# Performance work log

Hardware: AMD Instinct MI355X
Metric: run time of the kernel (lower is better)

The kernel has to match this reference:

```python
import jax, jax.numpy as jnp
import numpy as np

N_EMBD = 768

def setup_inputs() -> dict:
    key = jax.random.key(0)
    k1, k2, k3, k4 = jax.random.split(key, 4)
    B, T, head_size = 16, 1024, 128
    x = jax.random.normal(k1, (B, T, N_EMBD), dtype=jnp.float32)
    # nn.Linear(in, out, bias=False): weight stored as (out, in); we store transposed (in, out)
    s = 1.0 / np.sqrt(N_EMBD)
    Wk = jax.random.uniform(k2, (N_EMBD, head_size), jnp.float32, -s, s)
    Wq = jax.random.uniform(k3, (N_EMBD, head_size), jnp.float32, -s, s)
    Wv = jax.random.uniform(k4, (N_EMBD, head_size), jnp.float32, -s, s)
    return {"x": x, "Wk": Wk, "Wq": Wq, "Wv": Wv}

def reference(x, Wk, Wq, Wv):
    B, T, C = x.shape  # C == n_embd == 768
    k = jnp.einsum('btc,ch->bth', x, Wk)
    q = jnp.einsum('btc,ch->bth', x, Wq)
    v = jnp.einsum('btc,ch->bth', x, Wv)
    # NOTE: original scales by C**-0.5 with C = n_embd (768), not head_size.
    wei = jnp.einsum('bth,bsh->bts', q, k) * (C ** -0.5)  # (B, T, T)
    causal = jnp.tril(jnp.ones((T, T), dtype=bool))
    wei = jnp.where(causal, wei, -jnp.inf)
    wei = jax.nn.softmax(wei, axis=-1)
    # dropout p=0.0 -> identity
    return jnp.einsum('bts,bsh->bth', wei, v)
```

## Files before the change

kernel.cpp:

```cpp
#include <hip/hip_runtime.h>
#include <math.h>

#define NTOK   16384
#define NEMBD  768
#define HDIM   128

typedef __attribute__((ext_vector_type(8)))  short short8;
typedef __attribute__((ext_vector_type(16))) float floatx16;

#define MFMA32(a,b,c) __builtin_amdgcn_mfma_f32_32x32x16_bf16(a,b,c,0,0,0)

__device__ __forceinline__ unsigned short f2bf(float f) {
    unsigned u = __float_as_uint(f);
    u += 0x7fff + ((u >> 16) & 1);
    return (unsigned short)(u >> 16);
}
__device__ __forceinline__ unsigned pack2(float a, float b) {
    return (unsigned)f2bf(a) | ((unsigned)f2bf(b) << 16);
}
__device__ __forceinline__ unsigned pack2_trunc(float a, float b) {
    return __builtin_amdgcn_perm(__float_as_uint(b), __float_as_uint(a),
                                 0x07060302u);
}
__device__ __forceinline__ void gl_lds16(const void* gptr, void* lptr) {
    __builtin_amdgcn_global_load_lds(
        (const __attribute__((address_space(1))) unsigned int*)gptr,
        (__attribute__((address_space(3))) unsigned int*)lptr, 16, 0, 0);
}

__global__ __launch_bounds__(256) void prep_w(
    const float* __restrict__ Wk, const float* __restrict__ Wq,
    const float* __restrict__ Wv, unsigned short* __restrict__ wt)
{
    __shared__ float T[64 * 65];

    const int tid = threadIdx.x;
    const int bw  = blockIdx.x / 24;
    const int rem = blockIdx.x % 24;
    const int ct  = rem >> 1, dh = rem & 1;
    const int c0  = ct * 64, d0 = dh * 64;
    const float* W = (bw == 0) ? Wk : ((bw == 1) ? Wq : Wv);
    const float scale = (bw == 1)
        ? (0.03608439182435161f * 1.4426950408889634f) : 1.0f;

    #pragma unroll
    for (int pass = 0; pass < 4; ++pass) {
        int idx = pass * 256 + tid;
        int c  = idx >> 4;
        int d4 = idx & 15;
        float4 v = ((const float4*)W)[(size_t)(c0 + c) * 32 + dh * 16 + d4];
        v.x *= scale; v.y *= scale; v.z *= scale; v.w *= scale;
        T[(d4 * 4 + 0) * 65 + c] = v.x;
        T[(d4 * 4 + 1) * 65 + c] = v.y;
        T[(d4 * 4 + 2) * 65 + c] = v.z;
        T[(d4 * 4 + 3) * 65 + c] = v.w;
    }
    __syncthreads();

    #pragma unroll
    for (int pass = 0; pass < 2; ++pass) {
        int idx = pass * 256 + tid;
        int d  = idx >> 3;
        int c8 = idx & 7;
        const float* row = &T[d * 65 + c8 * 8];
        uint4 u = make_uint4(pack2(row[0], row[1]), pack2(row[2], row[3]),
                             pack2(row[4], row[5]), pack2(row[6], row[7]));
        *(uint4*)&wt[(size_t)bw * (HDIM * NEMBD) + (size_t)(d0 + d) * NEMBD
                     + c0 + c8 * 8] = u;
    }
}

__global__ __launch_bounds__(256) void qkv_fused(
    const float* __restrict__ x, const unsigned short* __restrict__ wt,
    unsigned short* __restrict__ kb, unsigned short* __restrict__ qb,
    unsigned short* __restrict__ vT)
{
    __shared__ __align__(16) char As[2][8192];
    __shared__ __align__(16) char Bs[2][24576];

    const int tid = threadIdx.x, w = tid >> 6, lane = tid & 63;
    const int l31 = lane & 31, h = lane >> 5;
    const int r8 = lane >> 3, c8 = lane & 7;
    const int wm = w >> 1, wn = w & 1;
    const int mtile = blockIdx.x >> 1, nh = blockIdx.x & 1;
    const int m0 = mtile * 64;
    const int nbase = nh * 192;
    const int arow = tid >> 2, ac = tid & 3;

    floatx16 acc[3];
    #pragma unroll
    for (int j = 0; j < 3; ++j)
        #pragma unroll
        for (int i = 0; i < 16; ++i) acc[j][i] = 0.f;

    const float* asrc = x + (size_t)(m0 + arow) * NEMBD + ac * 16;

    #pragma unroll
    for (int j = 0; j < 6; ++j) {
        int rowb = w * 48 + j * 8;
        int row  = rowb + r8;
        gl_lds16((const char*)wt + ((size_t)(nbase + row) * NEMBD) * 2
                     + ((c8 ^ (row & 7)) * 16),
                 Bs[0] + rowb * 128);
    }
    float4 a0 = ((const float4*)asrc)[0];
    float4 a1 = ((const float4*)asrc)[1];
    float4 a2 = ((const float4*)asrc)[2];
    float4 a3 = ((const float4*)asrc)[3];
    {
        uint4 u0 = make_uint4(pack2(a0.x, a0.y), pack2(a0.z, a0.w),
                              pack2(a1.x, a1.y), pack2(a1.z, a1.w));
        uint4 u1 = make_uint4(pack2(a2.x, a2.y), pack2(a2.z, a2.w),
                              pack2(a3.x, a3.y), pack2(a3.z, a3.w));
        int cA = 2 * ac, cB = 2 * ac + 1;
        *(uint4*)(As[0] + arow * 128 + ((cA ^ (arow & 7)) * 16)) = u0;
        *(uint4*)(As[0] + arow * 128 + ((cB ^ (arow & 7)) * 16)) = u1;
    }
    {
        const float4* src = (const float4*)(asrc + 64);
        a0 = src[0]; a1 = src[1]; a2 = src[2]; a3 = src[3];
    }
    __syncthreads();

    #pragma unroll
    for (int it = 0; it < 12; ++it) {
        char* Acur = As[it & 1];
        char* Bcur = Bs[it & 1];
        char* Anxt = As[(it & 1) ^ 1];
        char* Bnxt = Bs[(it & 1) ^ 1];

        if (it < 11) {
            const int k0n = (it + 1) * 64;
            #pragma unroll
            for (int j = 0; j < 6; ++j) {
                int rowb = w * 48 + j * 8;
                int row  = rowb + r8;
                gl_lds16((const char*)wt
                             + ((size_t)(nbase + row) * NEMBD + k0n) * 2
                             + ((c8 ^ (row & 7)) * 16),
                         Bnxt + rowb * 128);
            }
        }

        #pragma unroll
        for (int ks = 0; ks < 4; ++ks) {
            int ar = wm * 32 + l31;
            short8 af = *(const short8*)(Acur + ar * 128
                                         + (((2*ks + h) ^ (ar & 7)) * 16));
            #pragma unroll
            for (int j = 0; j < 3; ++j) {
                int br = wn * 96 + j * 32 + l31;
                short8 bf = *(const short8*)(Bcur + br * 128
                                             + (((2*ks + h) ^ (br & 7)) * 16));
                acc[j] = MFMA32(af, bf, acc[j]);
            }
        }

        if (it < 11) {
            uint4 u0 = make_uint4(pack2(a0.x, a0.y), pack2(a0.z, a0.w),
                                  pack2(a1.x, a1.y), pack2(a1.z, a1.w));
            uint4 u1 = make_uint4(pack2(a2.x, a2.y), pack2(a2.z, a2.w),
                                  pack2(a3.x, a3.y), pack2(a3.z, a3.w));
            int cA = 2 * ac, cB = 2 * ac + 1;
            *(uint4*)(Anxt + arow * 128 + ((cA ^ (arow & 7)) * 16)) = u0;
            *(uint4*)(Anxt + arow * 128 + ((cB ^ (arow & 7)) * 16)) = u1;
            if (it < 10) {
                const float4* src = (const float4*)(asrc + (it + 2) * 64);
                a0 = src[0]; a1 = src[1]; a2 = src[2]; a3 = src[3];
            }
        }
        __syncthreads();
    }

    const int tbase = m0 + wm * 32;
    #pragma unroll
    for (int j = 0; j < 3; ++j) {
        int n0 = nbase + wn * 96 + j * 32;
        if (n0 < 256) {
            unsigned short* outp = (n0 < 128) ? kb : qb;
            int d = (n0 & 127) + l31;
            #pragma unroll
            for (int r = 0; r < 16; ++r) {
                int t = tbase + (r & 3) + 8 * (r >> 2) + 4 * h;
                outp[(size_t)t * HDIM + d] = f2bf(acc[j][r]);
            }
        } else {
            int d = (n0 - 256) + l31, b = m0 >> 10, tloc = (m0 & 1023) + wm * 32;
            #pragma unroll
            for (int g = 0; g < 4; ++g) {
                int t = tloc + 8 * g + 4 * h;
                uint2 u = make_uint2(pack2(acc[j][4*g+0], acc[j][4*g+1]),
                                     pack2(acc[j][4*g+2], acc[j][4*g+3]));
                *(uint2*)((char*)vT + (((size_t)(b * HDIM + d)) * 1024 + t) * 2) = u;
            }
        }
    }
}

__global__ __launch_bounds__(256) void attn_mfma(
    const unsigned short* __restrict__ qb, const unsigned short* __restrict__ kb,
    const unsigned short* __restrict__ vT, float* __restrict__ out)
{
    __shared__ __align__(16) float Obuf[4 * 32 * 128];
    __shared__ float lred[128];

    const int tid = threadIdx.x, w = tid >> 6, lane = tid & 63;
    const int l31 = lane & 31, h = lane >> 5;
    const int u  = blockIdx.x & 255;
    const int b  = u & 15, p = u >> 4;
    const int qt = (blockIdx.x >> 8) ? (31 - p) : p;

    const char* kb_b = (const char*)kb + (size_t)b * (1024 * 256);
    const char* qb_b = (const char*)qb + (size_t)b * (1024 * 256);
    const char* vT_b = (const char*)vT + (size_t)b * (HDIM * 2048);

    short8 qf[8];
    {
        const char* qrow = qb_b + (size_t)(qt * 32 + l31) * 256 + h * 16;
        #pragma unroll
        for (int ks = 0; ks < 8; ++ks)
            qf[ks] = *(const short8*)(qrow + ks * 32);
    }

    floatx16 o[4];
    #pragma unroll
    for (int nt = 0; nt < 4; ++nt)
        #pragma unroll
        for (int i = 0; i < 16; ++i) o[nt][i] = 0.f;
    float l_r = 0.f;

    short8 kf[8];
    if (w <= qt) {
        const char* krow = kb_b + (size_t)(w * 32 + l31) * 256 + h * 16;
        #pragma unroll
        for (int ks = 0; ks < 8; ++ks)
            kf[ks] = *(const short8*)(krow + ks * 32);
    }

    for (int st = w; st <= qt; st += 4) {
        short8 vf[8];
        {
            const char* vrow0 = vT_b + (size_t)l31 * 2048 + (size_t)st * 64 + h * 16;
            #pragma unroll
            for (int nt = 0; nt < 4; ++nt) {
                const char* vr = vrow0 + (size_t)nt * (32 * 2048);
                vf[nt * 2 + 0] = *(const short8*)(vr + 0);
                vf[nt * 2 + 1] = *(const short8*)(vr + 32);
            }
        }
        floatx16 s;
        #pragma unroll
        for (int i = 0; i < 16; ++i) s[i] = 0.f;
        __builtin_amdgcn_s_setprio(1);
        #pragma unroll
        for (int ks = 0; ks < 8; ++ks) s = MFMA32(kf[ks], qf[ks], s);
        __builtin_amdgcn_s_setprio(0);

        if (st + 4 <= qt) {
            const char* krow = kb_b + (size_t)((st + 4) * 32 + l31) * 256 + h * 16;
            #pragma unroll
            for (int ks = 0; ks < 8; ++ks)
                kf[ks] = *(const short8*)(krow + ks * 32);
        }

        if (st == qt) {
            #pragma unroll
            for (int r = 0; r < 16; ++r) {
                int key = (r & 3) + 8 * (r >> 2) + 4 * h;
                if (key > l31) s[r] = -1e30f;
            }
        }
        float p16[16];
        float ps0 = 0.f, ps1 = 0.f, ps2 = 0.f, ps3 = 0.f;
        #pragma unroll
        for (int r = 0; r < 4; ++r) {
            p16[4*r+0] = __builtin_amdgcn_exp2f(s[4*r+0]);
            p16[4*r+1] = __builtin_amdgcn_exp2f(s[4*r+1]);
            p16[4*r+2] = __builtin_amdgcn_exp2f(s[4*r+2]);
            p16[4*r+3] = __builtin_amdgcn_exp2f(s[4*r+3]);
            ps0 += p16[4*r+0]; ps1 += p16[4*r+1];
            ps2 += p16[4*r+2]; ps3 += p16[4*r+3];
        }
        l_r += (ps0 + ps1) + (ps2 + ps3);

        unsigned own[8];
        #pragma unroll
        for (int i = 0; i < 8; ++i) own[i] = pack2_trunc(p16[2*i], p16[2*i+1]);
        asm("v_permlane32_swap_b32 %0, %1" : "+v"(own[0]), "+v"(own[2]));
        asm("v_permlane32_swap_b32 %0, %1" : "+v"(own[1]), "+v"(own[3]));
        asm("v_permlane32_swap_b32 %0, %1" : "+v"(own[4]), "+v"(own[6]));
        asm("v_permlane32_swap_b32 %0, %1" : "+v"(own[5]), "+v"(own[7]));
        short8 pf[2];
        {
            union { short8 v; unsigned uu[4]; } f0, f1;
            f0.uu[0]=own[0]; f0.uu[1]=own[1]; f0.uu[2]=own[2]; f0.uu[3]=own[3];
            f1.uu[0]=own[4]; f1.uu[1]=own[5]; f1.uu[2]=own[6]; f1.uu[3]=own[7];
            pf[0] = f0.v; pf[1] = f1.v;
        }
        __builtin_amdgcn_s_setprio(1);
        #pragma unroll
        for (int nt = 0; nt < 4; ++nt) {
            o[nt] = MFMA32(vf[nt * 2 + 0], pf[0], o[nt]);
            o[nt] = MFMA32(vf[nt * 2 + 1], pf[1], o[nt]);
        }
        __builtin_amdgcn_s_setprio(0);
    }

    l_r += __shfl_xor(l_r, 32, 64);
    if (lane < 32) lred[w * 32 + l31] = l_r;
    {
        float* mybuf = &Obuf[w * 4096];
        #pragma unroll
        for (int nt = 0; nt < 4; ++nt) {
            #pragma unroll
            for (int g = 0; g < 4; ++g) {
                int chunk = nt * 8 + 2 * g + h;
                int slot  = (chunk & 24) | ((chunk & 7) ^ (l31 & 7));
                *((float4*)&mybuf[l31 * 128] + slot) =
                    make_float4(o[nt][4*g+0], o[nt][4*g+1],
                                o[nt][4*g+2], o[nt][4*g+3]);
            }
        }
    }
    __syncthreads();
    {
        int q  = tid >> 3;
        int cb = (tid & 7) * 4;
        float inv = 1.f / (lred[q] + lred[32 + q] + lred[64 + q] + lred[96 + q]);
        #pragma unroll
        for (int cc = 0; cc < 4; ++cc) {
            int chunk = cb + cc;
            int slot  = (chunk & 24) | ((chunk & 7) ^ (q & 7));
            float4 v0 = *((float4*)&Obuf[0 * 4096 + q * 128] + slot);
            float4 v1 = *((float4*)&Obuf[1 * 4096 + q * 128] + slot);
            float4 v2 = *((float4*)&Obuf[2 * 4096 + q * 128] + slot);
            float4 v3 = *((float4*)&Obuf[3 * 4096 + q * 128] + slot);
            float4 v = make_float4((v0.x + v1.x + v2.x + v3.x) * inv,
                                   (v0.y + v1.y + v2.y + v3.y) * inv,
                                   (v0.z + v1.z + v2.z + v3.z) * inv,
                                   (v0.w + v1.w + v2.w + v3.w) * inv);
            *(float4*)&out[((size_t)(b * 1024 + qt * 32 + q)) * HDIM + chunk * 4] = v;
        }
    }
}

extern "C" void kernel_launch(void* const* d_in, const int* in_sizes, int n_in,
                              void* d_out, int out_size, void* d_ws, size_t ws_size,
                              hipStream_t stream)
{
    const float* x  = (const float*)d_in[0];
    const float* Wk = (const float*)d_in[1];
    const float* Wq = (const float*)d_in[2];
    const float* Wv = (const float*)d_in[3];
    float* outp = (float*)d_out;

    char* ws = (char*)d_ws;
    unsigned short* wt = (unsigned short*)(ws);
    unsigned short* kb = (unsigned short*)(ws + 589824);
    unsigned short* qb = (unsigned short*)(ws + 4784128);
    unsigned short* vT = (unsigned short*)(ws + 8978432);

    prep_w<<<72, 256, 0, stream>>>(Wk, Wq, Wv, wt);
    qkv_fused<<<512, 256, 0, stream>>>(x, wt, kb, qb, vT);
    attn_mfma<<<512, 256, 0, stream>>>(qb, kb, vT, outp);
}
```

Baseline: 125.3 us.

## Load x fragments directly into registers, bypassing LDS staging in QKV GEMM

The QKV projection kernel no longer stages the fp32 x tile through shared memory. Each lane now loads its own MFMA A-fragment straight from global memory into registers, one k-step ahead, and converts it to bf16 in place. This removes the LDS writes and reads for A and frees 16KB of shared memory per block. In exchange, two waves (wn=0/1) now redundantly load the same x rows from global memory, and more registers are in use. pack2 also switches to the HIP bf16x2 intrinsic.

```diff
diff --git a/kernel.cpp b/kernel.cpp
--- a/kernel.cpp
+++ b/kernel.cpp
@@ -1,4 +1,5 @@
 #include <hip/hip_runtime.h>
+#include <hip/hip_bf16.h>
 #include <math.h>
 
 #define NTOK   16384
@@ -16,7 +17,9 @@
     return (unsigned short)(u >> 16);
 }
 __device__ __forceinline__ unsigned pack2(float a, float b) {
-    return (unsigned)f2bf(a) | ((unsigned)f2bf(b) << 16);
+    __hip_bfloat162 h2 = __float22bfloat162_rn(make_float2(a, b));
+    union { __hip_bfloat162 h; unsigned u; } c; c.h = h2;
+    return c.u;
 }
 __device__ __forceinline__ unsigned pack2_trunc(float a, float b) {
     return __builtin_amdgcn_perm(__float_as_uint(b), __float_as_uint(a),
@@ -75,7 +78,6 @@
     unsigned short* __restrict__ kb, unsigned short* __restrict__ qb,
     unsigned short* __restrict__ vT)
 {
-    __shared__ __align__(16) char As[2][8192];
     __shared__ __align__(16) char Bs[2][24576];
 
     const int tid = threadIdx.x, w = tid >> 6, lane = tid & 63;
@@ -85,7 +87,6 @@
     const int mtile = blockIdx.x >> 1, nh = blockIdx.x & 1;
     const int m0 = mtile * 64;
     const int nbase = nh * 192;
-    const int arow = tid >> 2, ac = tid & 3;
 
     floatx16 acc[3];
     #pragma unroll
@@ -93,7 +94,8 @@
         #pragma unroll
         for (int i = 0; i < 16; ++i) acc[j][i] = 0.f;
 
-    const float* asrc = x + (size_t)(m0 + arow) * NEMBD + ac * 16;
+    const float4* xrow = (const float4*)(x + (size_t)(m0 + wm * 32 + l31) * NEMBD)
+                         + 2 * h;
 
     #pragma unroll
     for (int j = 0; j < 6; ++j) {
@@ -103,30 +105,17 @@
                      + ((c8 ^ (row & 7)) * 16),
                  Bs[0] + rowb * 128);
     }
-    float4 a0 = ((const float4*)asrc)[0];
-    float4 a1 = ((const float4*)asrc)[1];
-    float4 a2 = ((const float4*)asrc)[2];
-    float4 a3 = ((const float4*)asrc)[3];
-    {
-        uint4 u0 = make_uint4(pack2(a0.x, a0.y), pack2(a0.z, a0.w),
-                              pack2(a1.x, a1.y), pack2(a1.z, a1.w));
-        uint4 u1 = make_uint4(pack2(a2.x, a2.y), pack2(a2.z, a2.w),
-                              pack2(a3.x, a3.y), pack2(a3.z, a3.w));
-        int cA = 2 * ac, cB = 2 * ac + 1;
-        *(uint4*)(As[0] + arow * 128 + ((cA ^ (arow & 7)) * 16)) = u0;
-        *(uint4*)(As[0] + arow * 128 + ((cB ^ (arow & 7)) * 16)) = u1;
-    }
-    {
-        const float4* src = (const float4*)(asrc + 64);
-        a0 = src[0]; a1 = src[1]; a2 = src[2]; a3 = src[3];
+    float4 xa[8];
+    #pragma unroll
+    for (int ks = 0; ks < 4; ++ks) {
+        xa[2 * ks + 0] = xrow[4 * ks + 0];
+        xa[2 * ks + 1] = xrow[4 * ks + 1];
     }
     __syncthreads();
 
     #pragma unroll
     for (int it = 0; it < 12; ++it) {
-        char* Acur = As[it & 1];
         char* Bcur = Bs[it & 1];
-        char* Anxt = As[(it & 1) ^ 1];
         char* Bnxt = Bs[(it & 1) ^ 1];
 
         if (it < 11) {
@@ -142,31 +131,33 @@
             }
         }
 
+        short8 af[4];
         #pragma unroll
         for (int ks = 0; ks < 4; ++ks) {
-            int ar = wm * 32 + l31;
-            short8 af = *(const short8*)(Acur + ar * 128
-                                         + (((2*ks + h) ^ (ar & 7)) * 16));
+            union { short8 v; unsigned u[4]; } t;
+            t.u[0] = pack2(xa[2*ks+0].x, xa[2*ks+0].y);
+            t.u[1] = pack2(xa[2*ks+0].z, xa[2*ks+0].w);
+            t.u[2] = pack2(xa[2*ks+1].x, xa[2*ks+1].y);
+            t.u[3] = pack2(xa[2*ks+1].z, xa[2*ks+1].w);
+            af[ks] = t.v;
+        }
+        if (it < 11) {
+            const float4* xn = xrow + (it + 1) * 16;
+            #pragma unroll
+            for (int ks = 0; ks < 4; ++ks) {
+                xa[2 * ks + 0] = xn[4 * ks + 0];
+                xa[2 * ks + 1] = xn[4 * ks + 1];
+            }
+        }
+
+        #pragma unroll
+        for (int ks = 0; ks < 4; ++ks) {
             #pragma unroll
             for (int j = 0; j < 3; ++j) {
                 int br = wn * 96 + j * 32 + l31;
                 short8 bf = *(const short8*)(Bcur + br * 128
                                              + (((2*ks + h) ^ (br & 7)) * 16));
-                acc[j] = MFMA32(af, bf, acc[j]);
-            }
-        }
-
-        if (it < 11) {
-            uint4 u0 = make_uint4(pack2(a0.x, a0.y), pack2(a0.z, a0.w),
-                                  pack2(a1.x, a1.y), pack2(a1.z, a1.w));
-            uint4 u1 = make_uint4(pack2(a2.x, a2.y), pack2(a2.z, a2.w),
-                                  pack2(a3.x, a3.y), pack2(a3.z, a3.w));
-            int cA = 2 * ac, cB = 2 * ac + 1;
-            *(uint4*)(Anxt + arow * 128 + ((cA ^ (arow & 7)) * 16)) = u0;
-            *(uint4*)(Anxt + arow * 128 + ((cB ^ (arow & 7)) * 16)) = u1;
-            if (it < 10) {
-                const float4* src = (const float4*)(asrc + (it + 2) * 64);
-                a0 = src[0]; a1 = src[1]; a2 = src[2]; a3 = src[3];
+                acc[j] = MFMA32(af[ks], bf, acc[j]);
             }
         }
         __syncthreads();
```

Measured after the change: 143.5 us. 1.15x slower.
